# Kernel tuning notes

Hardware: AMD Instinct MI355X
Metric: run time of the kernel (lower is better)

The kernel has to match this reference:

```python
import jax, jax.numpy as jnp
import numpy as np

N, T, C, H = 512, 64, 64, 4
HD = C // H
FE = 4  # forward_expansion
EPS = 1e-5


def _p(key, shape, scale=0.05):
    return jax.random.normal(key, shape, dtype=jnp.float32) * scale


def setup_inputs() -> dict:
    key = jax.random.key(0)
    ks = jax.random.split(key, 24)
    return {
        'value': jax.random.normal(ks[0], (N, T, C), dtype=jnp.float32),
        'key_t': jax.random.normal(ks[1], (N, T, C), dtype=jnp.float32),
        'query': jax.random.normal(ks[2], (N, T, C), dtype=jnp.float32),
        'adj': jax.random.uniform(ks[3], (N, N), dtype=jnp.float32),
        # SSelfAttention params (nn.Linear weights, applied as x @ W.T)
        'Wv': _p(ks[4], (HD, HD)), 'Wk': _p(ks[5], (HD, HD)), 'Wq': _p(ks[6], (HD, HD)),
        'Wo': _p(ks[7], (C, C)), 'bo': jnp.zeros((C,), jnp.float32),
        # LayerNorms
        'g1': jnp.ones((C,), jnp.float32), 'b1': jnp.zeros((C,), jnp.float32),
        'g2': jnp.ones((C,), jnp.float32), 'b2': jnp.zeros((C,), jnp.float32),
        # FFN
        'Wf1': _p(ks[8], (FE * C, C)), 'bf1': jnp.zeros((FE * C,), jnp.float32),
        'Wf2': _p(ks[9], (C, FE * C)), 'bf2': jnp.zeros((C,), jnp.float32),
        # GCN (two GraphConvolution layers: adj @ (x @ W) + b, ReLU between)
        'Wg1': _p(ks[10], (C, C)), 'bg1': jnp.zeros((C,), jnp.float32),
        'Wg2': _p(ks[11], (C, C)), 'bg2': jnp.zeros((C,), jnp.float32),
        # gating linears
        'Wo1': _p(ks[12], (C, C)), 'bo1': jnp.zeros((C,), jnp.float32),
        'Wo2': _p(ks[13], (C, C)), 'bo2': jnp.zeros((C,), jnp.float32),
    }


def _layernorm(x, g, b):
    m = jnp.mean(x, axis=-1, keepdims=True)
    v = jnp.mean((x - m) ** 2, axis=-1, keepdims=True)
    return (x - m) * jax.lax.rsqrt(v + EPS) * g + b


def reference(value, key_t, query, adj, Wv, Wk, Wq, Wo, bo, g1, b1, g2, b2,
              Wf1, bf1, Wf2, bf2, Wg1, bg1, Wg2, bg2, Wo1, bo1, Wo2, bo2):
    n, t, c = query.shape
    # --- SSelfAttention: attention across nodes (q/k axes are nodes) ---
    vh = value.reshape(n, t, H, HD) @ Wv.T
    kh = key_t.reshape(n, t, H, HD) @ Wk.T
    qh = query.reshape(n, t, H, HD) @ Wq.T
    energy = jnp.einsum('qthd,kthd->qkth', qh, kh)  # [N,N,T,H]
    att = jax.nn.softmax(energy / jnp.sqrt(jnp.float32(c)), axis=1)
    attn_out = jnp.einsum('qkth,kthd->qthd', att, vh).reshape(n, t, c)
    attn_out = attn_out @ Wo.T + bo
    # --- residual + norm + FFN + norm (dropout = identity, eval mode) ---
    x = _layernorm(attn_out + query, g1, b1)
    ffn = jax.nn.relu(x @ Wf1.T + bf1) @ Wf2.T + bf2
    out1 = _layernorm(ffn + x, g2, b2)
    # --- InstanceNorm2d(1) on adj: normalize over whole NxN map (no affine) ---
    am = jnp.mean(adj)
    av = jnp.mean((adj - am) ** 2)
    adj_n = (adj - am) * jax.lax.rsqrt(av + EPS)
    # --- GCN applied per-timestep, vectorized over T ---
    h = jax.nn.relu(jnp.einsum('nm,mtc->ntc', adj_n, query @ Wg1.T) + bg1)
    out2 = jnp.einsum('nm,mtc->ntc', adj_n, h @ Wg2.T) + bg2
    # --- gated fusion ---
    g = jax.nn.sigmoid(out1 @ Wo1.T + bo1 + out2 @ Wo2.T + bo2)
    return g * out1 + (1.0 - g) * out2
```

## Files before the change

kernel.cpp:

```cpp
#include <hip/hip_runtime.h>

#define LN_EPS 1e-5f

typedef __attribute__((ext_vector_type(4))) short short4v;
typedef __attribute__((ext_vector_type(4))) float float4v;

__device__ __forceinline__ float wave_sum(float v) {
#pragma unroll
  for (int o = 32; o > 0; o >>= 1) v += __shfl_xor(v, o, 64);
  return v;
}

__device__ __forceinline__ unsigned short f2b(float f) {
  unsigned int u = __float_as_uint(f);
  u += 0x7fffu + ((u >> 16) & 1u);
  return (unsigned short)(u >> 16);
}

__device__ __forceinline__ float b2f(unsigned short h) {
  return __uint_as_float(((unsigned int)h) << 16);
}

__device__ __forceinline__ float4v mfma_16x16x16_bf16(short4v a, short4v b,
                                                      float4v c) {
#if __has_builtin(__builtin_amdgcn_mfma_f32_16x16x16bf16_1k)
  return __builtin_amdgcn_mfma_f32_16x16x16bf16_1k(a, b, c, 0, 0, 0);
#else
  float4v d;
  asm volatile(
      "v_mfma_f32_16x16x16_bf16 %0, %1, %2, %3\n\ts_nop 7\n\ts_nop 7"
      : "=v"(d)
      : "v"(a), "v"(b), "v"(c));
  return d;
#endif
}

__global__ __launch_bounds__(256) void s1_kernel(
    const float* __restrict__ adj, float* __restrict__ ps,
    float* __restrict__ pss, const float* __restrict__ value,
    const float* __restrict__ keyt, const float* __restrict__ query,
    const float* __restrict__ Wv, const float* __restrict__ Wk,
    const float* __restrict__ Wq, unsigned short* __restrict__ vt,
    unsigned short* __restrict__ kh, unsigned short* __restrict__ qh) {
  __shared__ float r1[4], r2[4];
  __shared__ __align__(16) float wv[256], wk[256], wq[256];
  const int b = blockIdx.x, tid = threadIdx.x;
  if (b < 512) {
    float v0 = adj[b * 512 + tid], v1 = adj[b * 512 + 256 + tid];
    float s = v0 + v1;
    float ss = fmaf(v0, v0, v1 * v1);
    s = wave_sum(s);
    ss = wave_sum(ss);
    if ((tid & 63) == 0) { r1[tid >> 6] = s; r2[tid >> 6] = ss; }
    __syncthreads();
    if (tid == 0) {
      ps[b] = r1[0] + r1[1] + r1[2] + r1[3];
      pss[b] = r2[0] + r2[1] + r2[2] + r2[3];
    }
  } else {
    wv[tid] = Wv[tid];
    wk[tid] = Wk[tid];
    wq[tid] = Wq[tid] * 0.125f;
    __syncthreads();
    const int th = b - 512;
    const int t = th >> 2, h = th & 3;
    const int base = t * 64 + h * 16;
    float y[16];
    unsigned short tmp[16];

#define XFORM(SRC, WARR)                                            \
  {                                                                 \
    const float4* p = (const float4*)(SRC + n * 4096 + base);       \
    float x[16];                                                    \
    *(float4*)(x + 0) = p[0];                                       \
    *(float4*)(x + 4) = p[1];                                       \
    *(float4*)(x + 8) = p[2];                                       \
    *(float4*)(x + 12) = p[3];                                      \
    _Pragma("unroll") for (int d = 0; d < 16; ++d) {                \
      float acc = 0.f;                                              \
      _Pragma("unroll") for (int e4 = 0; e4 < 4; ++e4) {            \
        float4 w4 = *(const float4*)&WARR[d * 16 + e4 * 4];         \
        acc = fmaf(w4.x, x[e4 * 4 + 0], acc);                       \
        acc = fmaf(w4.y, x[e4 * 4 + 1], acc);                       \
        acc = fmaf(w4.z, x[e4 * 4 + 2], acc);                       \
        acc = fmaf(w4.w, x[e4 * 4 + 3], acc);                       \
      }                                                             \
      y[d] = acc;                                                   \
    }                                                               \
  }

    for (int s = 0; s < 2; ++s) {
      const int n = tid + (s << 8);
      XFORM(value, wv)
#pragma unroll
      for (int d = 0; d < 16; ++d) vt[th * 8192 + d * 512 + n] = f2b(y[d]);
      XFORM(keyt, wk)
#pragma unroll
      for (int d = 0; d < 16; ++d) tmp[d] = f2b(y[d]);
      *(int4*)&kh[(th * 512 + n) * 16] = *(int4*)&tmp[0];
      *(int4*)&kh[(th * 512 + n) * 16 + 8] = *(int4*)&tmp[8];
      XFORM(query, wq)
#pragma unroll
      for (int d = 0; d < 16; ++d) tmp[d] = f2b(y[d]);
      *(int4*)&qh[(th * 512 + n) * 16] = *(int4*)&tmp[0];
      *(int4*)&qh[(th * 512 + n) * 16 + 8] = *(int4*)&tmp[8];
    }
#undef XFORM
  }
}

#define VPAD 536
__global__ __launch_bounds__(256) void s2_kernel(
    const float* __restrict__ adj, const float* __restrict__ ps,
    const float* __restrict__ pss, const float* __restrict__ query,
    const float* __restrict__ Wg1, const float* __restrict__ Wf1,
    const float* __restrict__ Wf2, const float* __restrict__ Wo1,
    const float* __restrict__ Wo2, const float* __restrict__ Wg2,
    const float* __restrict__ bg2, const float* __restrict__ bo1,
    const float* __restrict__ bo2, unsigned short* __restrict__ anh,
    unsigned short* __restrict__ anl, unsigned short* __restrict__ Yfh,
    unsigned short* __restrict__ Yfl, unsigned short* __restrict__ Wf1f,
    unsigned short* __restrict__ Wf2f, unsigned short* __restrict__ Wo1f,
    unsigned short* __restrict__ Wg2hf, unsigned short* __restrict__ Wg2lf,
    unsigned short* __restrict__ W32hf, unsigned short* __restrict__ W32lf,
    float* __restrict__ c2, const unsigned short* __restrict__ qh,
    const unsigned short* __restrict__ kh, const unsigned short* __restrict__ vt,
    float* __restrict__ o) {
  __shared__ float r1[4], r2[4];
  __shared__ __align__(16) char smem[33280];
  const int tid = threadIdx.x, b = blockIdx.x;
  if (b < 899) {
    float* pool = (float*)smem;
    if (b < 256) {
      float s = ps[tid] + ps[tid + 256];
      float ss = pss[tid] + pss[tid + 256];
      s = wave_sum(s);
      ss = wave_sum(ss);
      if ((tid & 63) == 0) { r1[tid >> 6] = s; r2[tid >> 6] = ss; }
      __syncthreads();
      const float sum = r1[0] + r1[1] + r1[2] + r1[3];
      const float sqs = r2[0] + r2[1] + r2[2] + r2[3];
      const float am = sum * (1.f / 262144.f);
      const float var = sqs * (1.f / 262144.f) - am * am;
      const float rs = rsqrtf(var + LN_EPS);
      const int i = (b * 256 + tid) * 4;
      float4 v = *(const float4*)&adj[i];
      float vals[4] = {(v.x - am) * rs, (v.y - am) * rs, (v.z - am) * rs,
                       (v.w - am) * rs};
      unsigned short th4[4], tl4[4];
#pragma unroll
      for (int j = 0; j < 4; ++j) {
        th4[j] = f2b(vals[j]);
        tl4[j] = f2b(vals[j] - b2f(th4[j]));
      }
      *(short4v*)&anh[i] = *(short4v*)th4;
      *(short4v*)&anl[i] = *(short4v*)tl4;
    } else if (b < 320) {
      const int id = (b - 256) * 256 + tid;
      const int n = id >> 6, k = id & 63;
      Wf1f[((k >> 4) * 256 + n) * 16 + (k & 15)] = f2b(Wf1[id]);
    } else if (b < 384) {
      const int id = (b - 320) * 256 + tid;
      const int n = id >> 8, k = id & 255;
      Wf2f[((k >> 4) * 64 + n) * 16 + (k & 15)] = f2b(Wf2[id]);
    } else if (b < 896) {
      const int pb = b - 384;
      const int w = tid >> 6, lane = tid & 63;
      const int mt = pb & 31;
      const int t = (pb >> 5) * 4 + w;
      float* xs = pool;
      float* Ls = pool + 256;
      float wc[64];
#pragma unroll
      for (int e = 0; e < 16; ++e)
        *(float4*)&wc[e * 4] = *(const float4*)&Wg1[lane * 64 + e * 4];
#pragma unroll 4
      for (int ms = 0; ms < 16; ++ms) {
        const int r = (mt * 16 + ms) * 64 + t;
        xs[w * 64 + lane] = query[r * 64 + lane];
        float acc = 0.f;
#pragma unroll
        for (int e = 0; e < 64; ++e) acc = fmaf(xs[w * 64 + e], wc[e], acc);
        Ls[(w * 16 + ms) * 68 + lane] = acc;
      }
      unsigned int dh[8], dl[8];
#pragma unroll
      for (int j = 0; j < 8; ++j) {
        float v0 = Ls[(w * 16 + 2 * j) * 68 + lane];
        float v1 = Ls[(w * 16 + 2 * j + 1) * 68 + lane];
        unsigned int h0 = f2b(v0), h1 = f2b(v1);
        unsigned int l0 = f2b(v0 - b2f((unsigned short)h0));
        unsigned int l1 = f2b(v1 - b2f((unsigned short)h1));
        dh[j] = h0 | (h1 << 16);
        dl[j] = l0 | (l1 << 16);
      }
      const int off = ((mt * 4096) + t * 64 + lane) * 16;
      *(uint4*)(Yfh + off) = *(uint4*)&dh[0];
      *(uint4*)(Yfh + off + 8) = *(uint4*)&dh[4];
      *(uint4*)(Yfl + off) = *(uint4*)&dl[0];
      *(uint4*)(Yfl + off + 8) = *(uint4*)&dl[4];
    } else if (b == 896) {
      for (int i = tid; i < 4096; i += 256) {
        const int n = i >> 6, k = i & 63;
        Wo1f[((k >> 4) * 64 + n) * 16 + (k & 15)] = f2b(Wo1[i]);
      }
    } else if (b == 897) {
      for (int i = tid; i < 4096; i += 256) {
        const int n = i >> 6, k = i & 63;
        const float v = Wg2[i];
        const unsigned short h = f2b(v);
        const unsigned short l = f2b(v - b2f(h));
        Wg2hf[((k >> 4) * 64 + n) * 16 + (k & 15)] = h;
        Wg2lf[((k >> 4) * 64 + n) * 16 + (k & 15)] = l;
      }
    } else {
      float* wo2s = pool;
      float* wg2s = pool + 4096;
      float* bg2s = pool + 8192;
      for (int i = tid; i < 4096; i += 256) {
        wo2s[i] = Wo2[i];
        wg2s[i] = Wg2[i];
      }
      if (tid < 64) bg2s[tid] = bg2[tid];
      __syncthreads();
#pragma unroll 4
      for (int t = 0; t < 16; ++t) {
        const int i = t * 256 + tid;
        const int r = i >> 6, c = i & 63;
        float acc = 0.f;
#pragma unroll
        for (int e = 0; e < 64; ++e)
          acc = fmaf(wo2s[r * 64 + e], wg2s[e * 64 + c], acc);
        const unsigned short h = f2b(acc);
        const unsigned short l = f2b(acc - b2f(h));
        W32hf[((c >> 4) * 64 + r) * 16 + (c & 15)] = h;
        W32lf[((c >> 4) * 64 + r) * 16 + (c & 15)] = l;
      }
      if (tid < 64) {
        float acc = bo1[tid] + bo2[tid];
#pragma unroll
        for (int e = 0; e < 64; ++e)
          acc = fmaf(wo2s[tid * 64 + e], bg2s[e], acc);
        c2[tid] = acc;
      }
    }
  } else {
    unsigned short* Vs = (unsigned short*)smem;
    const int bx = b - 899;
    const int th = bx >> 2;
    {
      const unsigned short* vb = vt + th * 8192;
#pragma unroll
      for (int it = 0; it < 4; ++it) {
        const int flat = (it * 256 + tid) * 8;
        const int d = flat >> 9, k = flat & 511;
        *(int4*)&Vs[d * VPAD + k] = *(const int4*)&vb[flat];
      }
    }
    __syncthreads();

    const int lane = tid & 15;
    const int quad = (tid >> 4) & 3;
    const int w = tid >> 6;
    const int q0 = (bx & 3) * 128 + w * 32;

    const unsigned short* qbase = qh + th * 8192;
    const unsigned short* kbase = kh + th * 8192;
    short4v qf[2];
#pragma unroll
    for (int ct = 0; ct < 2; ++ct)
      qf[ct] = *(const short4v*)&qbase[(q0 + ct * 16 + lane) * 16 + quad * 4];

    float4v acc[2];
    float l[2];
#pragma unroll
    for (int ct = 0; ct < 2; ++ct) {
      acc[ct].x = 0.f; acc[ct].y = 0.f; acc[ct].z = 0.f; acc[ct].w = 0.f;
      l[ct] = 0.f;
    }
    float4v zero;
    zero.x = 0.f; zero.y = 0.f; zero.z = 0.f; zero.w = 0.f;

    const unsigned short* vrow = &Vs[lane * VPAD];

    for (int kt = 0; kt < 32; ++kt) {
      const short4v kf =
          *(const short4v*)&kbase[(kt * 16 + lane) * 16 + quad * 4];
      const short4v vf = *(const short4v*)&vrow[kt * 16 + quad * 4];
#pragma unroll
      for (int ct = 0; ct < 2; ++ct) {
        float4v s = mfma_16x16x16_bf16(kf, qf[ct], zero);
        float p0 = __expf(s.x);
        float p1 = __expf(s.y);
        float p2 = __expf(s.z);
        float p3 = __expf(s.w);
        l[ct] += (p0 + p1) + (p2 + p3);
        unsigned int u0 = __float_as_uint(p0) + 0x8000u;
        unsigned int u1 = __float_as_uint(p1) + 0x8000u;
        unsigned int u2 = __float_as_uint(p2) + 0x8000u;
        unsigned int u3 = __float_as_uint(p3) + 0x8000u;
        union {
          uint2 u;
          short4v s4;
        } pk;
        pk.u.x = __builtin_amdgcn_perm(u1, u0, 0x07060302u);
        pk.u.y = __builtin_amdgcn_perm(u3, u2, 0x07060302u);
        acc[ct] = mfma_16x16x16_bf16(vf, pk.s4, acc[ct]);
      }
    }

#pragma unroll
    for (int ct = 0; ct < 2; ++ct) {
      float lt = l[ct];
      lt += __shfl_xor(lt, 16, 64);
      lt += __shfl_xor(lt, 32, 64);
      const float inv = 1.f / lt;
      float4 out;
      out.x = acc[ct].x * inv;
      out.y = acc[ct].y * inv;
      out.z = acc[ct].z * inv;
      out.w = acc[ct].w * inv;
      const int q = q0 + ct * 16 + lane;
      *(float4*)&o[th * 8192 + q * 16 + quad * 4] = out;
    }
  }
}

__global__ __launch_bounds__(256) void s3_kernel(
    const float* __restrict__ o, const float* __restrict__ query,
    const float* __restrict__ Wo, const float* __restrict__ bo,
    const float* __restrict__ g1, const float* __restrict__ b1,
    const unsigned short* __restrict__ Wf1f, const float* __restrict__ bf1,
    const unsigned short* __restrict__ Wf2f, const float* __restrict__ bf2,
    const float* __restrict__ g2, const float* __restrict__ b2,
    float* __restrict__ out1, unsigned short* __restrict__ out1b,
    const unsigned short* __restrict__ Ah, const unsigned short* __restrict__ Al,
    const unsigned short* __restrict__ Bh, const unsigned short* __restrict__ Bl,
    const float* __restrict__ bg1, unsigned short* __restrict__ Hh,
    unsigned short* __restrict__ Hl) {
  __shared__ __align__(16) char smem[60416];
  const int tid = threadIdx.x, b = blockIdx.x;
  const int w = tid >> 6, lane = tid & 63;
  const int ln = lane & 15, quad = lane >> 4;
  if (b < 512) {
    float* xs_res = (float*)smem;
    unsigned short* xb = (unsigned short*)(smem + 17408);
    unsigned short* hid = (unsigned short*)(smem + 26112);
    float* bcast = (float*)(smem + 59392);
    const int n = b;
    {
      float wc[64];
#pragma unroll
      for (int e = 0; e < 16; ++e)
        *(float4*)&wc[e * 4] = *(const float4*)&Wo[lane * 64 + e * 4];
      const float boc = bo[lane], gc = g1[lane], bc1 = b1[lane];
      const int hsel = lane >> 4, dsel = lane & 15;
      for (int i = 0; i < 16; ++i) {
        const int tt = w * 16 + i;
        bcast[w * 64 + lane] = o[(tt * 4 + hsel) * 8192 + n * 16 + dsel];
        float acc = 0.f;
#pragma unroll
        for (int e = 0; e < 64; ++e) acc = fmaf(bcast[w * 64 + e], wc[e], acc);
        float y = acc + boc + query[(n * 64 + tt) * 64 + lane];
        float mean = wave_sum(y) * 0.015625f;
        float d = y - mean;
        float var = wave_sum(d * d) * 0.015625f;
        float v = d * rsqrtf(var + LN_EPS) * gc + bc1;
        xs_res[tt * 68 + lane] = v;
        xb[tt * 68 + lane] = f2b(v);
      }
    }
    __syncthreads();

    {
      const int wm = (w & 1) * 32, wn = (w >> 1) * 128;
      float4v acc[2][8];
#pragma unroll
      for (int i = 0; i < 2; ++i)
#pragma unroll
        for (int j = 0; j < 8; ++j) {
          acc[i][j].x = 0.f; acc[i][j].y = 0.f;
          acc[i][j].z = 0.f; acc[i][j].w = 0.f;
        }
#pragma unroll
      for (int kt = 0; kt < 4; ++kt) {
        short4v a0 = *(const short4v*)&xb[(wm + ln) * 68 + kt * 16 + quad * 4];
        short4v a1 =
            *(const short4v*)&xb[(wm + 16 + ln) * 68 + kt * 16 + quad * 4];
#pragma unroll
        for (int j = 0; j < 8; ++j) {
          short4v bfr = *(const short4v*)&Wf1f[(kt * 256 + wn + j * 16 + ln) *
                                                   16 + quad * 4];
          acc[0][j] = mfma_16x16x16_bf16(a0, bfr, acc[0][j]);
          acc[1][j] = mfma_16x16x16_bf16(a1, bfr, acc[1][j]);
        }
      }
#pragma unroll
      for (int mt = 0; mt < 2; ++mt)
#pragma unroll
        for (int j = 0; j < 8; ++j) {
          const int col = wn + j * 16 + ln;
          const float bb = bf1[col];
#pragma unroll
          for (int reg = 0; reg < 4; ++reg) {
            const int row = wm + mt * 16 + quad * 4 + reg;
            hid[row * 260 + col] = f2b(fmaxf(acc[mt][j][reg] + bb, 0.f));
          }
        }
    }
    __syncthreads();

    {
      float4v acc[4];
#pragma unroll
      for (int j = 0; j < 4; ++j) {
        acc[j].x = 0.f; acc[j].y = 0.f; acc[j].z = 0.f; acc[j].w = 0.f;
      }
#pragma unroll 4
      for (int kt = 0; kt < 16; ++kt) {
        short4v a =
            *(const short4v*)&hid[(w * 16 + ln) * 260 + kt * 16 + quad * 4];
#pragma unroll
        for (int j = 0; j < 4; ++j) {
          short4v bfr =
              *(const short4v*)&Wf2f[(kt * 64 + j * 16 + ln) * 16 + quad * 4];
          acc[j] = mfma_16x16x16_bf16(a, bfr, acc[j]);
        }
      }
#pragma unroll
      for (int reg = 0; reg < 4; ++reg) {
        const int row = w * 16 + quad * 4 + reg;
        float v[4];
        float s = 0.f;
#pragma unroll
        for (int j = 0; j < 4; ++j) {
          v[j] = acc[j][reg] + bf2[j * 16 + ln] + xs_res[row * 68 + j * 16 + ln];
          s += v[j];
        }
        s += __shfl_xor(s, 1, 64);
        s += __shfl_xor(s, 2, 64);
        s += __shfl_xor(s, 4, 64);
        s += __shfl_xor(s, 8, 64);
        const float mean = s * 0.015625f;
        float vv = 0.f;
#pragma unroll
        for (int j = 0; j < 4; ++j) {
          const float dd = v[j] - mean;
          vv += dd * dd;
        }
        vv += __shfl_xor(vv, 1, 64);
        vv += __shfl_xor(vv, 2, 64);
        vv += __shfl_xor(vv, 4, 64);
        vv += __shfl_xor(vv, 8, 64);
        const float rs = rsqrtf(vv * 0.015625f + LN_EPS);
#pragma unroll
        for (int j = 0; j < 4; ++j) {
          const float ov =
              (v[j] - mean) * rs * g2[j * 16 + ln] + b2[j * 16 + ln];
          const int idx = (n * 64 + row) * 64 + j * 16 + ln;
          out1[idx] = ov;
          out1b[idx] = f2b(ov);
        }
      }
    }
  } else {
    const int pb = b - 512;
    const int wave = w;
    const int wm = (wave & 1) * 32, wn = (wave >> 1) * 64;
    const int m0 = (pb >> 5) * 64 + wm;
    const int n0 = (pb & 31) * 128 + wn;

    const unsigned short* ah0 = Ah + (m0 + ln) * 512 + quad * 4;
    const unsigned short* al0 = Al + (m0 + ln) * 512 + quad * 4;
    const unsigned short* bh0 = Bh + (n0 + ln) * 16 + quad * 4;
    const unsigned short* bl0 = Bl + (n0 + ln) * 16 + quad * 4;

    float4v acc[2][4];
#pragma unroll
    for (int i = 0; i < 2; ++i)
#pragma unroll
      for (int j = 0; j < 4; ++j) {
        acc[i][j].x = 0.f; acc[i][j].y = 0.f;
        acc[i][j].z = 0.f; acc[i][j].w = 0.f;
      }

#pragma unroll 2
    for (int kt = 0; kt < 32; ++kt) {
      short4v a0h = *(const short4v*)(ah0 + kt * 16);
      short4v a1h = *(const short4v*)(ah0 + 16 * 512 + kt * 16);
      short4v a0l = *(const short4v*)(al0 + kt * 16);
      short4v a1l = *(const short4v*)(al0 + 16 * 512 + kt * 16);
#pragma unroll
      for (int j = 0; j < 4; ++j) {
        const int boff = (kt * 4096 + j * 16) * 16;
        short4v bh = *(const short4v*)(bh0 + boff);
        short4v bl = *(const short4v*)(bl0 + boff);
        acc[0][j] = mfma_16x16x16_bf16(a0l, bh, acc[0][j]);
        acc[0][j] = mfma_16x16x16_bf16(a0h, bl, acc[0][j]);
        acc[0][j] = mfma_16x16x16_bf16(a0h, bh, acc[0][j]);
        acc[1][j] = mfma_16x16x16_bf16(a1l, bh, acc[1][j]);
        acc[1][j] = mfma_16x16x16_bf16(a1h, bl, acc[1][j]);
        acc[1][j] = mfma_16x16x16_bf16(a1h, bh, acc[1][j]);
      }
    }

#pragma unroll
    for (int mt = 0; mt < 2; ++mt) {
      const int mtile = (m0 + mt * 16) >> 4;
#pragma unroll
      for (int j = 0; j < 4; ++j) {
        const int col = n0 + j * 16 + ln;
        const float bb = bg1[col & 63];
        unsigned short hh[4], hl[4];
#pragma unroll
        for (int reg = 0; reg < 4; ++reg) {
          float v = fmaxf(acc[mt][j][reg] + bb, 0.f);
          hh[reg] = f2b(v);
          hl[reg] = f2b(v - b2f(hh[reg]));
        }
        const int off = (mtile * 4096 + col) * 16 + quad * 4;
        *(uint2*)&Hh[off] = *(uint2*)hh;
        *(uint2*)&Hl[off] = *(uint2*)hl;
      }
    }
  }
}

__global__ __launch_bounds__(256) void s4_kernel(
    const unsigned short* __restrict__ Ah, const unsigned short* __restrict__ Al,
    const unsigned short* __restrict__ Bh, const unsigned short* __restrict__ Bl,
    unsigned short* __restrict__ G2h, unsigned short* __restrict__ G2l) {
  const int tid = threadIdx.x;
  const int wave = tid >> 6, lane = tid & 63;
  const int ln = lane & 15, quad = lane >> 4;
  const int wm = (wave & 1) * 32, wn = (wave >> 1) * 32;
  const int m0 = (blockIdx.x >> 6) * 64 + wm;
  const int n0 = (blockIdx.x & 63) * 64 + wn;

  const unsigned short* ah0 = Ah + (m0 + ln) * 512 + quad * 4;
  const unsigned short* al0 = Al + (m0 + ln) * 512 + quad * 4;
  const unsigned short* bh0 = Bh + (n0 + ln) * 16 + quad * 4;
  const unsigned short* bl0 = Bl + (n0 + ln) * 16 + quad * 4;

  float4v acc[2][2];
#pragma unroll
  for (int i = 0; i < 2; ++i)
#pragma unroll
    for (int j = 0; j < 2; ++j) {
      acc[i][j].x = 0.f; acc[i][j].y = 0.f;
      acc[i][j].z = 0.f; acc[i][j].w = 0.f;
    }

#pragma unroll 4
  for (int kt = 0; kt < 32; ++kt) {
    short4v a0h = *(const short4v*)(ah0 + kt * 16);
    short4v a1h = *(const short4v*)(ah0 + 16 * 512 + kt * 16);
    short4v a0l = *(const short4v*)(al0 + kt * 16);
    short4v a1l = *(const short4v*)(al0 + 16 * 512 + kt * 16);
#pragma unroll
    for (int j = 0; j < 2; ++j) {
      const int boff = (kt * 4096 + j * 16) * 16;
      short4v bh = *(const short4v*)(bh0 + boff);
      short4v bl = *(const short4v*)(bl0 + boff);
      acc[0][j] = mfma_16x16x16_bf16(a0l, bh, acc[0][j]);
      acc[0][j] = mfma_16x16x16_bf16(a0h, bl, acc[0][j]);
      acc[0][j] = mfma_16x16x16_bf16(a0h, bh, acc[0][j]);
      acc[1][j] = mfma_16x16x16_bf16(a1l, bh, acc[1][j]);
      acc[1][j] = mfma_16x16x16_bf16(a1h, bl, acc[1][j]);
      acc[1][j] = mfma_16x16x16_bf16(a1h, bh, acc[1][j]);
    }
  }

#pragma unroll
  for (int mt = 0; mt < 2; ++mt)
#pragma unroll
    for (int j = 0; j < 2; ++j) {
      const int col = n0 + j * 16 + ln;
#pragma unroll
      for (int reg = 0; reg < 4; ++reg) {
        const int row = m0 + mt * 16 + quad * 4 + reg;
        const float v = acc[mt][j][reg];
        const unsigned short h = f2b(v);
        G2h[row * 4096 + col] = h;
        G2l[row * 4096 + col] = f2b(v - b2f(h));
      }
    }
}

__global__ __launch_bounds__(256) void s5_kernel(
    const unsigned short* __restrict__ out1b, const float* __restrict__ out1,
    const unsigned short* __restrict__ G2h, const unsigned short* __restrict__ G2l,
    const unsigned short* __restrict__ Wo1f, const unsigned short* __restrict__ Wg2hf,
    const unsigned short* __restrict__ Wg2lf, const unsigned short* __restrict__ W32hf,
    const unsigned short* __restrict__ W32lf, const float* __restrict__ bg2,
    const float* __restrict__ c2, float* __restrict__ dst) {
  const int tid = threadIdx.x;
  const int wave = tid >> 6, lane = tid & 63;
  const int ln = lane & 15, quad = lane >> 4;
  const int m0 = blockIdx.x * 64 + wave * 16;

  const unsigned short* o1p = out1b + (m0 + ln) * 64 + quad * 4;
  const unsigned short* ghp = G2h + (m0 + ln) * 64 + quad * 4;
  const unsigned short* glp = G2l + (m0 + ln) * 64 + quad * 4;

  float4v aco[4], aca[4];
#pragma unroll
  for (int j = 0; j < 4; ++j) {
    aco[j].x = 0.f; aco[j].y = 0.f; aco[j].z = 0.f; aco[j].w = 0.f;
    aca[j].x = 0.f; aca[j].y = 0.f; aca[j].z = 0.f; aca[j].w = 0.f;
  }

#pragma unroll
  for (int kt = 0; kt < 4; ++kt) {
    const short4v ao = *(const short4v*)(o1p + kt * 16);
    const short4v gh = *(const short4v*)(ghp + kt * 16);
    const short4v gl = *(const short4v*)(glp + kt * 16);
#pragma unroll
    for (int j = 0; j < 4; ++j) {
      const int boff = (kt * 64 + j * 16 + ln) * 16 + quad * 4;
      const short4v wgh = *(const short4v*)(Wg2hf + boff);
      const short4v wgl = *(const short4v*)(Wg2lf + boff);
      const short4v wo1 = *(const short4v*)(Wo1f + boff);
      const short4v w3h = *(const short4v*)(W32hf + boff);
      const short4v w3l = *(const short4v*)(W32lf + boff);
      aco[j] = mfma_16x16x16_bf16(gl, wgh, aco[j]);
      aco[j] = mfma_16x16x16_bf16(gh, wgl, aco[j]);
      aco[j] = mfma_16x16x16_bf16(gh, wgh, aco[j]);
      aca[j] = mfma_16x16x16_bf16(ao, wo1, aca[j]);
      aca[j] = mfma_16x16x16_bf16(gl, w3h, aca[j]);
      aca[j] = mfma_16x16x16_bf16(gh, w3l, aca[j]);
      aca[j] = mfma_16x16x16_bf16(gh, w3h, aca[j]);
    }
  }

#pragma unroll
  for (int j = 0; j < 4; ++j) {
    const int col = j * 16 + ln;
    const float bg2v = bg2[col];
    const float c2v = c2[col];
#pragma unroll
    for (int reg = 0; reg < 4; ++reg) {
      const int row = m0 + quad * 4 + reg;
      const float o2 = aco[j][reg] + bg2v;
      const float a = aca[j][reg] + c2v;
      const float o1v = out1[row * 64 + col];
      const float g = 1.f / (1.f + __expf(-a));
      dst[row * 64 + col] = o2 + g * (o1v - o2);
    }
  }
}

extern "C" void kernel_launch(void* const* d_in, const int* in_sizes, int n_in,
                              void* d_out, int out_size, void* d_ws,
                              size_t ws_size, hipStream_t stream) {
  const float* value = (const float*)d_in[0];
  const float* key_t = (const float*)d_in[1];
  const float* query = (const float*)d_in[2];
  const float* adj = (const float*)d_in[3];
  const float* Wv = (const float*)d_in[4];
  const float* Wk = (const float*)d_in[5];
  const float* Wq = (const float*)d_in[6];
  const float* Wo = (const float*)d_in[7];
  const float* bo = (const float*)d_in[8];
  const float* g1 = (const float*)d_in[9];
  const float* b1 = (const float*)d_in[10];
  const float* g2 = (const float*)d_in[11];
  const float* b2 = (const float*)d_in[12];
  const float* Wf1 = (const float*)d_in[13];
  const float* bf1 = (const float*)d_in[14];
  const float* Wf2 = (const float*)d_in[15];
  const float* bf2 = (const float*)d_in[16];
  const float* Wg1 = (const float*)d_in[17];
  const float* bg1 = (const float*)d_in[18];
  const float* Wg2 = (const float*)d_in[19];
  const float* bg2 = (const float*)d_in[20];
  const float* Wo1 = (const float*)d_in[21];
  const float* bo1 = (const float*)d_in[22];
  const float* Wo2 = (const float*)d_in[23];
  const float* bo2 = (const float*)d_in[24];

  float* ws = (float*)d_ws;
  const size_t M1 = 1048576;
  float* o = ws + 0;
  float* out1 = ws + 2 * M1;
  unsigned short* out1b = (unsigned short*)(ws + 4 * M1);
  unsigned short* qh = (unsigned short*)(ws + 5 * M1);
  unsigned short* kh = (unsigned short*)(ws + 6 * M1);
  unsigned short* vt = (unsigned short*)(ws + 7 * M1);
  unsigned short* Yfh = (unsigned short*)(ws + 8 * M1);
  unsigned short* Yfl = (unsigned short*)(ws + 9 * M1);
  unsigned short* Hrfh = (unsigned short*)(ws + 10 * M1);
  unsigned short* Hrfl = (unsigned short*)(ws + 11 * M1);
  unsigned short* G2h = (unsigned short*)(ws + 12 * M1);
  unsigned short* G2l = (unsigned short*)(ws + 13 * M1);
  unsigned short* anh = (unsigned short*)(ws + 14 * M1);
  unsigned short* anl = (unsigned short*)(ws + 14 * M1 + 131072);
  float* wbase = ws + 14 * M1 + 262144;
  unsigned short* Wf1f = (unsigned short*)(wbase);
  unsigned short* Wf2f = (unsigned short*)(wbase + 8192);
  unsigned short* Wo1f = (unsigned short*)(wbase + 16384);
  unsigned short* Wg2hf = (unsigned short*)(wbase + 18432);
  unsigned short* Wg2lf = (unsigned short*)(wbase + 20480);
  unsigned short* W32hf = (unsigned short*)(wbase + 22528);
  unsigned short* W32lf = (unsigned short*)(wbase + 24576);
  float* c2 = wbase + 26624;
  float* ps = wbase + 26688;
  float* pss = ps + 512;
  float* dst = (float*)d_out;

  s1_kernel<<<768, 256, 0, stream>>>(adj, ps, pss, value, key_t, query, Wv,
                                     Wk, Wq, vt, kh, qh);
  s2_kernel<<<1923, 256, 0, stream>>>(adj, ps, pss, query, Wg1, Wf1, Wf2, Wo1,
                                      Wo2, Wg2, bg2, bo1, bo2, anh, anl, Yfh,
                                      Yfl, Wf1f, Wf2f, Wo1f, Wg2hf, Wg2lf,
                                      W32hf, W32lf, c2, qh, kh, vt, o);
  s3_kernel<<<768, 256, 0, stream>>>(o, query, Wo, bo, g1, b1, Wf1f, bf1,
                                     Wf2f, bf2, g2, b2, out1, out1b, anh, anl,
                                     Yfh, Yfl, bg1, Hrfh, Hrfl);
  s4_kernel<<<512, 256, 0, stream>>>(anh, anl, Hrfh, Hrfl, G2h, G2l);
  s5_kernel<<<512, 256, 0, stream>>>(out1b, out1, G2h, G2l, Wo1f, Wg2hf,
                                     Wg2lf, W32hf, W32lf, bg2, c2, dst);
}
```

Measured before the change: 277.1 us.

## Compute attention output projection with bf16 MFMA and node-major bf16 attention output

The attention kernel now writes its output in bf16, laid out node-major as [n][t][c], instead of fp32 head-major. A new s2 block pre-packs Wo into bf16 fragment layout. s3 then does the Wo projection with MFMA, replacing per-row scalar FMA through LDS broadcasts. The LayerNorm residual stays in registers instead of LDS, which cuts LDS use. This halves intermediate traffic and removes a slow scalar GEMM, at the cost of bf16 precision in the Wo projection input and weights.

```diff
diff --git a/kernel.cpp b/kernel.cpp
--- a/kernel.cpp
+++ b/kernel.cpp
@@ -116,20 +116,21 @@
     const float* __restrict__ Wg1, const float* __restrict__ Wf1,
     const float* __restrict__ Wf2, const float* __restrict__ Wo1,
     const float* __restrict__ Wo2, const float* __restrict__ Wg2,
-    const float* __restrict__ bg2, const float* __restrict__ bo1,
-    const float* __restrict__ bo2, unsigned short* __restrict__ anh,
-    unsigned short* __restrict__ anl, unsigned short* __restrict__ Yfh,
-    unsigned short* __restrict__ Yfl, unsigned short* __restrict__ Wf1f,
-    unsigned short* __restrict__ Wf2f, unsigned short* __restrict__ Wo1f,
-    unsigned short* __restrict__ Wg2hf, unsigned short* __restrict__ Wg2lf,
-    unsigned short* __restrict__ W32hf, unsigned short* __restrict__ W32lf,
+    const float* __restrict__ Wo, const float* __restrict__ bg2,
+    const float* __restrict__ bo1, const float* __restrict__ bo2,
+    unsigned short* __restrict__ anh, unsigned short* __restrict__ anl,
+    unsigned short* __restrict__ Yfh, unsigned short* __restrict__ Yfl,
+    unsigned short* __restrict__ Wf1f, unsigned short* __restrict__ Wf2f,
+    unsigned short* __restrict__ Wo1f, unsigned short* __restrict__ Wg2hf,
+    unsigned short* __restrict__ Wg2lf, unsigned short* __restrict__ W32hf,
+    unsigned short* __restrict__ W32lf, unsigned short* __restrict__ Wof,
     float* __restrict__ c2, const unsigned short* __restrict__ qh,
     const unsigned short* __restrict__ kh, const unsigned short* __restrict__ vt,
-    float* __restrict__ o) {
+    unsigned short* __restrict__ obf) {
   __shared__ float r1[4], r2[4];
   __shared__ __align__(16) char smem[33280];
   const int tid = threadIdx.x, b = blockIdx.x;
-  if (b < 899) {
+  if (b < 900) {
     float* pool = (float*)smem;
     if (b < 256) {
       float s = ps[tid] + ps[tid + 256];
@@ -213,7 +214,7 @@
         Wg2hf[((k >> 4) * 64 + n) * 16 + (k & 15)] = h;
         Wg2lf[((k >> 4) * 64 + n) * 16 + (k & 15)] = l;
       }
-    } else {
+    } else if (b == 898) {
       float* wo2s = pool;
       float* wg2s = pool + 4096;
       float* bg2s = pool + 8192;
@@ -243,10 +244,15 @@
           acc = fmaf(wo2s[tid * 64 + e], bg2s[e], acc);
         c2[tid] = acc;
       }
+    } else {
+      for (int i = tid; i < 4096; i += 256) {
+        const int n = i >> 6, k = i & 63;
+        Wof[((k >> 4) * 64 + n) * 16 + (k & 15)] = f2b(Wo[i]);
+      }
     }
   } else {
     unsigned short* Vs = (unsigned short*)smem;
-    const int bx = b - 899;
+    const int bx = b - 900;
     const int th = bx >> 2;
     {
       const unsigned short* vb = vt + th * 8192;
@@ -309,26 +315,27 @@
       }
     }
 
+    const int t = th >> 2, h = th & 3;
 #pragma unroll
     for (int ct = 0; ct < 2; ++ct) {
       float lt = l[ct];
       lt += __shfl_xor(lt, 16, 64);
       lt += __shfl_xor(lt, 32, 64);
       const float inv = 1.f / lt;
-      float4 out;
-      out.x = acc[ct].x * inv;
-      out.y = acc[ct].y * inv;
-      out.z = acc[ct].z * inv;
-      out.w = acc[ct].w * inv;
+      unsigned short tmp[4];
+      tmp[0] = f2b(acc[ct].x * inv);
+      tmp[1] = f2b(acc[ct].y * inv);
+      tmp[2] = f2b(acc[ct].z * inv);
+      tmp[3] = f2b(acc[ct].w * inv);
       const int q = q0 + ct * 16 + lane;
-      *(float4*)&o[th * 8192 + q * 16 + quad * 4] = out;
+      *(uint2*)&obf[(q * 64 + t) * 64 + h * 16 + quad * 4] = *(uint2*)tmp;
     }
   }
 }
 
 __global__ __launch_bounds__(256) void s3_kernel(
-    const float* __restrict__ o, const float* __restrict__ query,
-    const float* __restrict__ Wo, const float* __restrict__ bo,
+    const unsigned short* __restrict__ obf, const float* __restrict__ query,
+    const unsigned short* __restrict__ Wof, const float* __restrict__ bo,
     const float* __restrict__ g1, const float* __restrict__ b1,
     const unsigned short* __restrict__ Wf1f, const float* __restrict__ bf1,
     const unsigned short* __restrict__ Wf2f, const float* __restrict__ bf2,
@@ -338,36 +345,67 @@
     const unsigned short* __restrict__ Bh, const unsigned short* __restrict__ Bl,
     const float* __restrict__ bg1, unsigned short* __restrict__ Hh,
     unsigned short* __restrict__ Hl) {
-  __shared__ __align__(16) char smem[60416];
+  __shared__ __align__(16) char smem[41984];
   const int tid = threadIdx.x, b = blockIdx.x;
   const int w = tid >> 6, lane = tid & 63;
   const int ln = lane & 15, quad = lane >> 4;
   if (b < 512) {
-    float* xs_res = (float*)smem;
-    unsigned short* xb = (unsigned short*)(smem + 17408);
-    unsigned short* hid = (unsigned short*)(smem + 26112);
-    float* bcast = (float*)(smem + 59392);
+    unsigned short* xb = (unsigned short*)smem;
+    unsigned short* hid = (unsigned short*)(smem + 8704);
     const int n = b;
+    float xres[4][4];
+
     {
-      float wc[64];
-#pragma unroll
-      for (int e = 0; e < 16; ++e)
-        *(float4*)&wc[e * 4] = *(const float4*)&Wo[lane * 64 + e * 4];
-      const float boc = bo[lane], gc = g1[lane], bc1 = b1[lane];
-      const int hsel = lane >> 4, dsel = lane & 15;
-      for (int i = 0; i < 16; ++i) {
-        const int tt = w * 16 + i;
-        bcast[w * 64 + lane] = o[(tt * 4 + hsel) * 8192 + n * 16 + dsel];
-        float acc = 0.f;
-#pragma unroll
-        for (int e = 0; e < 64; ++e) acc = fmaf(bcast[w * 64 + e], wc[e], acc);
-        float y = acc + boc + query[(n * 64 + tt) * 64 + lane];
-        float mean = wave_sum(y) * 0.015625f;
-        float d = y - mean;
-        float var = wave_sum(d * d) * 0.015625f;
-        float v = d * rsqrtf(var + LN_EPS) * gc + bc1;
-        xs_res[tt * 68 + lane] = v;
-        xb[tt * 68 + lane] = f2b(v);
+      const unsigned short* ap = obf + (n * 64 + w * 16 + ln) * 64 + quad * 4;
+      float4v acc[4];
+#pragma unroll
+      for (int j = 0; j < 4; ++j) {
+        acc[j].x = 0.f; acc[j].y = 0.f; acc[j].z = 0.f; acc[j].w = 0.f;
+      }
+#pragma unroll
+      for (int kt = 0; kt < 4; ++kt) {
+        const short4v a = *(const short4v*)(ap + kt * 16);
+#pragma unroll
+        for (int j = 0; j < 4; ++j) {
+          const short4v bfr =
+              *(const short4v*)&Wof[(kt * 64 + j * 16 + ln) * 16 + quad * 4];
+          acc[j] = mfma_16x16x16_bf16(a, bfr, acc[j]);
+        }
+      }
+#pragma unroll
+      for (int reg = 0; reg < 4; ++reg) {
+        const int row = w * 16 + quad * 4 + reg;
+        float v[4];
+        float s = 0.f;
+#pragma unroll
+        for (int j = 0; j < 4; ++j) {
+          const int col = j * 16 + ln;
+          v[j] = acc[j][reg] + bo[col] + query[(n * 64 + row) * 64 + col];
+          s += v[j];
+        }
+        s += __shfl_xor(s, 1, 64);
+        s += __shfl_xor(s, 2, 64);
+        s += __shfl_xor(s, 4, 64);
+        s += __shfl_xor(s, 8, 64);
+        const float mean = s * 0.015625f;
+        float vv = 0.f;
+#pragma unroll
+        for (int j = 0; j < 4; ++j) {
+          const float dd = v[j] - mean;
+          vv += dd * dd;
+        }
+        vv += __shfl_xor(vv, 1, 64);
+        vv += __shfl_xor(vv, 2, 64);
+        vv += __shfl_xor(vv, 4, 64);
+        vv += __shfl_xor(vv, 8, 64);
+        const float rs = rsqrtf(vv * 0.015625f + LN_EPS);
+#pragma unroll
+        for (int j = 0; j < 4; ++j) {
+          const int col = j * 16 + ln;
+          const float xv = (v[j] - mean) * rs * g1[col] + b1[col];
+          xres[j][reg] = xv;
+          xb[row * 68 + col] = f2b(xv);
+        }
       }
     }
     __syncthreads();
@@ -434,7 +472,7 @@
         float s = 0.f;
 #pragma unroll
         for (int j = 0; j < 4; ++j) {
-          v[j] = acc[j][reg] + bf2[j * 16 + ln] + xs_res[row * 68 + j * 16 + ln];
+          v[j] = acc[j][reg] + bf2[j * 16 + ln] + xres[j][reg];
           s += v[j];
         }
         s += __shfl_xor(s, 1, 64);
@@ -681,7 +719,7 @@
 
   float* ws = (float*)d_ws;
   const size_t M1 = 1048576;
-  float* o = ws + 0;
+  unsigned short* obf = (unsigned short*)(ws + 0);
   float* out1 = ws + 2 * M1;
   unsigned short* out1b = (unsigned short*)(ws + 4 * M1);
   unsigned short* qh = (unsigned short*)(ws + 5 * M1);
@@ -703,18 +741,20 @@
   unsigned short* Wg2lf = (unsigned short*)(wbase + 20480);
   unsigned short* W32hf = (unsigned short*)(wbase + 22528);
   unsigned short* W32lf = (unsigned short*)(wbase + 24576);
-  float* c2 = wbase + 26624;
-  float* ps = wbase + 26688;
+  unsigned short* Wof = (unsigned short*)(wbase + 26624);
+  float* c2 = wbase + 28672;
+  float* ps = wbase + 28736;
   float* pss = ps + 512;
   float* dst = (float*)d_out;
 
   s1_kernel<<<768, 256, 0, stream>>>(adj, ps, pss, value, key_t, query, Wv,
                                      Wk, Wq, vt, kh, qh);
-  s2_kernel<<<1923, 256, 0, stream>>>(adj, ps, pss, query, Wg1, Wf1, Wf2, Wo1,
-                                      Wo2, Wg2, bg2, bo1, bo2, anh, anl, Yfh,
-                                      Yfl, Wf1f, Wf2f, Wo1f, Wg2hf, Wg2lf,
-                                      W32hf, W32lf, c2, qh, kh, vt, o);
-  s3_kernel<<<768, 256, 0, stream>>>(o, query, Wo, bo, g1, b1, Wf1f, bf1,
+  s2_kernel<<<1924, 256, 0, stream>>>(adj, ps, pss, query, Wg1, Wf1, Wf2, Wo1,
+                                      Wo2, Wg2, Wo, bg2, bo1, bo2, anh, anl,
+                                      Yfh, Yfl, Wf1f, Wf2f, Wo1f, Wg2hf,
+                                      Wg2lf, W32hf, W32lf, Wof, c2, qh, kh,
+                                      vt, obf);
+  s3_kernel<<<768, 256, 0, stream>>>(obf, query, Wof, bo, g1, b1, Wf1f, bf1,
                                      Wf2f, bf2, g2, b2, out1, out1b, anh, anl,
                                      Yfh, Yfl, bg1, Hrfh, Hrfl);
   s4_kernel<<<512, 256, 0, stream>>>(anh, anl, Hrfh, Hrfl, G2h, G2l);
```

Result: faster. 253.0 us (-8.7%).
